# Optimization experiments

Hardware: AMD Instinct MI355X
Metric: run time of the kernel (lower is better)

The kernel has to match this reference:

```python
import jax, jax.numpy as jnp
import numpy as np

N, L, NB, D, H, DH, IN, T = 128, 512, 4, 1024, 16, 64, 1024, 512


def setup_inputs() -> dict:
    key = jax.random.key(0)
    ks = iter(jax.random.split(key, 80))

    def nrm(shape, scale=1.0):
        return jax.random.normal(next(ks), shape, jnp.float32) * scale

    sD = 1.0 / float(np.sqrt(D))
    sH = 1.0 / float(np.sqrt(DH))
    inp = {
        "x": nrm((N, IN)),
        "memories": nrm((N, L, NB, D)),
        "mask": jnp.ones((N, L), jnp.int32),
        "memory_indices": jnp.sort(jax.random.randint(next(ks), (N, L), 0, T), axis=1),
        "max_episode_steps": T,
        "We": nrm((IN, D), sD), "be": jnp.zeros((D,), jnp.float32),
        "Wq": nrm((NB, H, DH, DH), sH), "Wk": nrm((NB, H, DH, DH), sH), "Wv": nrm((NB, H, DH, DH), sH),
        "Wo": nrm((NB, D, D), sD), "bo": jnp.zeros((NB, D), jnp.float32),
        "Wfc": nrm((NB, D, D), sD), "bfc": jnp.zeros((NB, D), jnp.float32),
        "ln1_g": jnp.ones((NB, D), jnp.float32), "ln1_b": jnp.zeros((NB, D), jnp.float32),
        "ln2_g": jnp.ones((NB, D), jnp.float32), "ln2_b": jnp.zeros((NB, D), jnp.float32),
        "lnkv_g": jnp.ones((NB, D), jnp.float32), "lnkv_b": jnp.zeros((NB, D), jnp.float32),
    }
    for g in ("g1", "g2"):
        for w in ("Wr", "Ur", "Wz", "Uz", "Wg", "Ug"):
            inp[g + "_" + w] = nrm((NB, D, D), sD)
        inp[g + "_bg"] = jnp.zeros((NB, D), jnp.float32)
    return inp


def _ln(x, g, b):
    m = jnp.mean(x, -1, keepdims=True)
    v = jnp.var(x, -1, keepdims=True)
    return (x - m) / jnp.sqrt(v + 1e-5) * g + b


def _gru(x, y, Wr, Ur, Wz, Uz, Wg, Ug, bg):
    # GTrXL GRU gate (swap_inputs=False): x = residual stream, y = sublayer output
    r = jax.nn.sigmoid(y @ Wr + x @ Ur)
    z = jax.nn.sigmoid(y @ Wz + x @ Uz - bg)
    h = jnp.tanh(y @ Wg + (r * x) @ Ug)
    return (1.0 - z) * x + z * h


def reference(x, memories, mask, memory_indices, max_episode_steps,
              We, be, Wq, Wk, Wv, Wo, bo, Wfc, bfc,
              ln1_g, ln1_b, ln2_g, ln2_b, lnkv_g, lnkv_b,
              g1_Wr, g1_Ur, g1_Wz, g1_Uz, g1_Wg, g1_Ug, g1_bg,
              g2_Wr, g2_Ur, g2_Wz, g2_Uz, g2_Wg, g2_Ug, g2_bg):
    d = We.shape[1]
    nb, nh, dh, _ = Wq.shape
    n, lm = mask.shape
    h = jax.nn.relu(x @ We + be)                        # (N, D) input embedding
    # relative sinusoidal positions (newest -> oldest), as in SinusoidalPosition
    inv = 10000.0 ** (-jnp.arange(0.0, d, 2.0) / d)     # (D/2,)
    seq = jnp.arange(max_episode_steps - 1, -1, -1.0)   # (T,)
    si = seq[:, None] * inv[None, :]
    pos = jnp.concatenate([jnp.sin(si), jnp.cos(si)], -1)   # (T, D)
    mem = memories + pos[memory_indices][:, :, None, :]     # (N, L, NB, D)
    maskb = (mask == 0)[:, None, None, :]               # (N,1,1,L)
    scale = 1.0 / jnp.sqrt(jnp.float32(d))
    layer_inputs = []
    att = None
    for i in range(nb):
        layer_inputs.append(jax.lax.stop_gradient(h))
        q = h[:, None, :]                                # (N,1,D) query length 1
        q_ = _ln(q, ln1_g[i], ln1_b[i])                  # pre-LN
        kv = _ln(mem[:, :, i], lnkv_g[i], lnkv_b[i])     # key = value (shared LN)
        qh = q_.reshape(n, 1, nh, dh)
        kh = kv.reshape(n, lm, nh, dh)
        Qp = jnp.einsum('nqhd,hde->nqhe', qh, Wq[i])     # per-head projections
        Kp = jnp.einsum('nkhd,hde->nkhe', kh, Wk[i])
        Vp = jnp.einsum('nkhd,hde->nkhe', kh, Wv[i])
        energy = jnp.einsum('nqhd,nkhd->nhqk', Qp, Kp)
        energy = jnp.where(maskb, jnp.float32(-1e20), energy)
        att = jax.nn.softmax(energy * scale, axis=-1)    # scaled by sqrt(embed_dim)
        ao = jnp.einsum('nhqk,nkhd->nqhd', att, Vp).reshape(n, 1, d)
        ao = ao @ Wo[i] + bo[i]
        h1 = _gru(q, ao, g1_Wr[i], g1_Ur[i], g1_Wz[i], g1_Uz[i], g1_Wg[i], g1_Ug[i], g1_bg[i])
        h_ = _ln(h1, ln2_g[i], ln2_b[i])
        fwd = jax.nn.relu(h_ @ Wfc[i] + bfc[i])
        h = _gru(h1, fwd, g2_Wr[i], g2_Ur[i], g2_Wz[i], g2_Uz[i], g2_Wg[i], g2_Ug[i], g2_bg[i])[:, 0]
    return h, jnp.stack(layer_inputs, axis=1)            # (N,D), (N,NB,D)
```

## Files before the change

kernel.cpp:

```cpp
#include <hip/hip_runtime.h>
#include <hip/hip_bf16.h>

#define N_   128
#define L_   512
#define NB_  4
#define D_   1024
#define H_   16
#define DH_  64
#define IN_  1024
#define T_   512

#define KS_  8
#define NCV_ 32

typedef __attribute__((ext_vector_type(8))) short short8v;
typedef __attribute__((ext_vector_type(4))) float float4v;

__device__ __forceinline__ short f2bf(float f) {
  unsigned u = __float_as_uint(f);
  u += 0x7FFFu + ((u >> 16) & 1u);
  return (short)(u >> 16);
}
__device__ __forceinline__ int pack2(float a, float b) {
  return (int)(unsigned short)f2bf(a) | ((int)f2bf(b) << 16);
}

__global__ __launch_bounds__(512) void pos_kernel(float* __restrict__ pos) {
  int t = blockIdx.x;
  int j = threadIdx.x;
  float seq = (float)(T_ - 1 - t);
  float ex  = (float)(2 * j) * (1.0f / (float)D_);
  float inv = expf(-ex * 9.210340371976184f);
  float si  = seq * inv;
  pos[(size_t)t * D_ + j]        = sinf(si);
  pos[(size_t)t * D_ + 512 + j]  = cosf(si);
}

#define LDK_ 136
template<int COLW, int NC, bool HAS2>
__global__ __launch_bounds__(256) void gemm_part_t(const float* __restrict__ A1,
                                                   const float* __restrict__ B1a,
                                                   const float* __restrict__ B1b,
                                                   const float* __restrict__ A2,
                                                   const float* __restrict__ B2a,
                                                   const float* __restrict__ B2b,
                                                   float* __restrict__ Cpart) {
  constexpr int KC = 128;
  constexpr int CT = COLW / 16;
  __shared__ short As[N_ * LDK_];
  __shared__ short Bs[COLW * LDK_];
  const int tid = threadIdx.x;
  const int colg0 = blockIdx.x * COLW;
  const int k0 = blockIdx.y * KC;
  const float* B1 = B1a;
  const float* B2 = B2a;
  int col0 = colg0;
  if (NC == 2048 && colg0 >= 1024) { B1 = B1b; B2 = B2b; col0 = colg0 - 1024; }

  const int wid  = tid >> 6;
  const int lane = tid & 63;
  const int lrow = lane & 15;
  const int lk8  = (lane >> 4) * 8;
  const int wrow0 = wid * 32;

  float4v acc[2][CT];
  #pragma unroll
  for (int a = 0; a < 2; ++a)
    #pragma unroll
    for (int b = 0; b < CT; ++b)
      acc[a][b] = (float4v){0.f, 0.f, 0.f, 0.f};

  const int arow  = tid >> 1;
  const int ahalf = (tid & 1) * 64;

  #pragma unroll
  for (int pass = 0; pass < (HAS2 ? 2 : 1); ++pass) {
    const float* A = pass ? A2 : A1;
    const float* B = pass ? B2 : B1;
    if (pass) __syncthreads();
    {
      const float* ap = &A[(size_t)arow * D_ + k0 + ahalf];
      short* dst = &As[arow * LDK_ + ahalf];
      #pragma unroll
      for (int j = 0; j < 16; ++j) {
        float4 v = *(const float4*)&ap[4 * j];
        *(int2*)&dst[4 * j] = make_int2(pack2(v.x, v.y), pack2(v.z, v.w));
      }
    }
    if (COLW == 64) {
      const int bcol = tid & 63, bkq = (tid >> 6) * 32;
      int regs[16];
      #pragma unroll
      for (int j = 0; j < 16; ++j) {
        float v0 = B[(size_t)(k0 + bkq + 2 * j) * D_ + col0 + bcol];
        float v1 = B[(size_t)(k0 + bkq + 2 * j + 1) * D_ + col0 + bcol];
        regs[j] = pack2(v0, v1);
      }
      short* dst = &Bs[bcol * LDK_ + bkq];
      *(int4*)&dst[0]  = make_int4(regs[0],  regs[1],  regs[2],  regs[3]);
      *(int4*)&dst[8]  = make_int4(regs[4],  regs[5],  regs[6],  regs[7]);
      *(int4*)&dst[16] = make_int4(regs[8],  regs[9],  regs[10], regs[11]);
      *(int4*)&dst[24] = make_int4(regs[12], regs[13], regs[14], regs[15]);
    } else {
      const int bcol = tid & 31, bkq = (tid >> 5) * 16;
      int regs[8];
      #pragma unroll
      for (int j = 0; j < 8; ++j) {
        float v0 = B[(size_t)(k0 + bkq + 2 * j) * D_ + col0 + bcol];
        float v1 = B[(size_t)(k0 + bkq + 2 * j + 1) * D_ + col0 + bcol];
        regs[j] = pack2(v0, v1);
      }
      short* dst = &Bs[bcol * LDK_ + bkq];
      *(int4*)&dst[0] = make_int4(regs[0], regs[1], regs[2], regs[3]);
      *(int4*)&dst[8] = make_int4(regs[4], regs[5], regs[6], regs[7]);
    }
    __syncthreads();
    #pragma unroll
    for (int kk = 0; kk < KC; kk += 32) {
      short8v a0 = *(const short8v*)&As[(wrow0 + lrow)      * LDK_ + kk + lk8];
      short8v a1 = *(const short8v*)&As[(wrow0 + 16 + lrow) * LDK_ + kk + lk8];
      #pragma unroll
      for (int ct = 0; ct < CT; ++ct) {
        short8v bf = *(const short8v*)&Bs[(ct * 16 + lrow) * LDK_ + kk + lk8];
        acc[0][ct] = __builtin_amdgcn_mfma_f32_16x16x32_bf16(a0, bf, acc[0][ct], 0, 0, 0);
        acc[1][ct] = __builtin_amdgcn_mfma_f32_16x16x32_bf16(a1, bf, acc[1][ct], 0, 0, 0);
      }
    }
  }
  float* Cp = &Cpart[(size_t)blockIdx.y * (N_ * NC)];
  const int crow = (lane >> 4) * 4;
  const int ccol = lane & 15;
  #pragma unroll
  for (int rt = 0; rt < 2; ++rt)
    #pragma unroll
    for (int ct = 0; ct < CT; ++ct)
      #pragma unroll
      for (int j = 0; j < 4; ++j) {
        int row = wrow0 + rt * 16 + crow + j;
        int col = colg0 + ct * 16 + ccol;
        Cp[(size_t)row * NC + col] = acc[rt][ct][j];
      }
}

__device__ __forceinline__ void ln_qk_epilogue(int n, const float* v4, int tid,
                                               const float* __restrict__ lg,
                                               const float* __restrict__ lb,
                                               const float* __restrict__ Wq,
                                               const float* __restrict__ Wk,
                                               float* __restrict__ qkb,
                                               float* qln, float* Qp) {
  int c = tid * 4;
  float s = v4[0] + v4[1] + v4[2] + v4[3];
  float q = v4[0]*v4[0] + v4[1]*v4[1] + v4[2]*v4[2] + v4[3]*v4[3];
  __shared__ float sa[4], sb[4];
  #pragma unroll
  for (int o = 32; o; o >>= 1) { s += __shfl_xor(s, o, 64); q += __shfl_xor(q, o, 64); }
  if ((tid & 63) == 0) { sa[tid >> 6] = s; sb[tid >> 6] = q; }
  __syncthreads();
  s = sa[0] + sa[1] + sa[2] + sa[3];
  q = sb[0] + sb[1] + sb[2] + sb[3];
  float mean = s * (1.f / D_);
  float var  = q * (1.f / D_) - mean * mean;
  float rstd = rsqrtf(var + 1e-5f);
  #pragma unroll
  for (int j = 0; j < 4; ++j)
    qln[c + j] = (v4[j] - mean) * rstd * lg[c + j] + lb[c + j];
  __syncthreads();
  #pragma unroll
  for (int j = 0; j < 4; ++j) {
    int idx = tid + j * 256; int h = idx >> 6, e = idx & 63;
    float acc = 0.f;
    for (int d = 0; d < DH_; ++d)
      acc += qln[(h << 6) + d] * Wq[((size_t)(h << 6) + d) * DH_ + e];
    Qp[idx] = acc;
  }
  __syncthreads();
  #pragma unroll
  for (int j = 0; j < 4; ++j) {
    int idx = tid + j * 256; int h = idx >> 6, d = idx & 63;
    float acc = 0.f;
    for (int e = 0; e < DH_; ++e)
      acc += Wk[((size_t)(h << 6) + d) * DH_ + e] * Qp[(h << 6) + e];
    qkb[(size_t)n * D_ + idx] = acc * 0.03125f;
  }
}

__global__ __launch_bounds__(256) void comb_embed_lnqk(const float* __restrict__ Cp,
                                                       const float* __restrict__ bias,
                                                       const float* __restrict__ lg,
                                                       const float* __restrict__ lb,
                                                       const float* __restrict__ Wq,
                                                       const float* __restrict__ Wk,
                                                       float* __restrict__ hcur,
                                                       float* __restrict__ out_li,
                                                       float* __restrict__ qkb) {
  int n = blockIdx.x, tid = threadIdx.x, c = tid * 4;
  __shared__ float qln[D_], Qp[D_];
  float4 a4 = {0.f, 0.f, 0.f, 0.f};
  #pragma unroll
  for (int s = 0; s < KS_; ++s) {
    float4 p = *(const float4*)&Cp[(size_t)s * (N_ * D_) + (size_t)n * D_ + c];
    a4.x += p.x; a4.y += p.y; a4.z += p.z; a4.w += p.w;
  }
  float4 b4 = *(const float4*)&bias[c];
  float v[4] = {fmaxf(a4.x + b4.x, 0.f), fmaxf(a4.y + b4.y, 0.f),
                fmaxf(a4.z + b4.z, 0.f), fmaxf(a4.w + b4.w, 0.f)};
  *(float4*)&hcur[(size_t)n * D_ + c] = *(float4*)v;
  *(float4*)&out_li[((size_t)n * NB_ + 0) * D_ + c] = *(float4*)v;
  ln_qk_epilogue(n, v, tid, lg, lb, Wq, Wk, qkb, qln, Qp);
}

__global__ __launch_bounds__(256) void attn_stream(
    const float* __restrict__ mem, const float* __restrict__ pos,
    const int* __restrict__ mask, const int* __restrict__ midx,
    const float* __restrict__ qkv, const float* __restrict__ lng,
    const float* __restrict__ lnb, int blk,
    float* __restrict__ pav, float* __restrict__ pm, float* __restrict__ ps)
{
  const int n    = blockIdx.y;
  const int w    = threadIdx.x >> 6;
  const int lane = threadIdx.x & 63;
  const int vc   = blockIdx.x * 4 + w;
  const int l0   = vc * (L_ / NCV_);
  const int d0   = lane * 16;

  float g[16], bv[16], qv[16];
  #pragma unroll
  for (int j = 0; j < 4; ++j) {
    float4 t0 = *(const float4*)&lng[d0 + 4 * j];
    g[4*j+0] = t0.x; g[4*j+1] = t0.y; g[4*j+2] = t0.z; g[4*j+3] = t0.w;
    float4 t1 = *(const float4*)&lnb[d0 + 4 * j];
    bv[4*j+0] = t1.x; bv[4*j+1] = t1.y; bv[4*j+2] = t1.z; bv[4*j+3] = t1.w;
    float4 t2 = *(const float4*)&qkv[(size_t)n * D_ + d0 + 4 * j];
    qv[4*j+0] = t2.x; qv[4*j+1] = t2.y; qv[4*j+2] = t2.z; qv[4*j+3] = t2.w;
  }
  float m_run = -INFINITY, s_run = 0.f;
  float av[16];
  #pragma unroll
  for (int j = 0; j < 16; ++j) av[j] = 0.f;

  for (int l = l0; l < l0 + (L_ / NCV_); ++l) {
    if (mask[(size_t)n * L_ + l] == 0) continue;
    const float* xr = &mem[(((size_t)n * L_ + l) * NB_ + blk) * D_ + d0];
    const int tt = midx[(size_t)n * L_ + l];
    const float* pr = &pos[(size_t)tt * D_ + d0];
    float xv[16];
    #pragma unroll
    for (int j = 0; j < 4; ++j) {
      float4 a = *(const float4*)&xr[4 * j];
      float4 p = *(const float4*)&pr[4 * j];
      xv[4*j+0] = a.x + p.x; xv[4*j+1] = a.y + p.y;
      xv[4*j+2] = a.z + p.z; xv[4*j+3] = a.w + p.w;
    }
    float s1 = 0.f, s2 = 0.f;
    #pragma unroll
    for (int j = 0; j < 16; ++j) { s1 += xv[j]; s2 += xv[j] * xv[j]; }
    #pragma unroll
    for (int o = 32; o; o >>= 1) { s1 += __shfl_xor(s1, o, 64); s2 += __shfl_xor(s2, o, 64); }
    float mean = s1 * (1.f / D_);
    float var  = s2 * (1.f / D_) - mean * mean;
    float rstd = rsqrtf(var + 1e-5f);
    float e = 0.f;
    float y[16];
    #pragma unroll
    for (int j = 0; j < 16; ++j) {
      y[j] = (xv[j] - mean) * rstd * g[j] + bv[j];
      e += y[j] * qv[j];
    }
    e += __shfl_xor(e, 1, 64);
    e += __shfl_xor(e, 2, 64);
    float mn = fmaxf(m_run, e);
    float al = __expf(m_run - mn);
    float pw = __expf(e - mn);
    s_run = s_run * al + pw;
    #pragma unroll
    for (int j = 0; j < 16; ++j) av[j] = av[j] * al + pw * y[j];
    m_run = mn;
  }
  size_t base = ((size_t)n * NCV_ + vc) * D_ + d0;
  #pragma unroll
  for (int j = 0; j < 16; ++j) pav[base + j] = av[j];
  if ((lane & 3) == 0) {
    size_t mb = ((size_t)n * NCV_ + vc) * H_ + (lane >> 2);
    pm[mb] = m_run;
    ps[mb] = s_run;
  }
}

__global__ __launch_bounds__(256) void attn_fin(const float* __restrict__ pav,
                                                const float* __restrict__ pm,
                                                const float* __restrict__ ps,
                                                const float* __restrict__ Wv,
                                                float* __restrict__ tb) {
  int n = blockIdx.x, tid = threadIdx.x;
  int d0 = tid * 4; int h = tid >> 4;
  float M = -INFINITY;
  for (int c = 0; c < NCV_; ++c) M = fmaxf(M, pm[((size_t)n * NCV_ + c) * H_ + h]);
  float S = 0.f, a0 = 0.f, a1 = 0.f, a2 = 0.f, a3 = 0.f;
  if (M > -INFINITY) {
    for (int c = 0; c < NCV_; ++c) {
      float mc = pm[((size_t)n * NCV_ + c) * H_ + h];
      if (mc == -INFINITY) continue;
      float wgt = __expf(mc - M);
      S += ps[((size_t)n * NCV_ + c) * H_ + h] * wgt;
      size_t ab = ((size_t)n * NCV_ + c) * D_ + d0;
      float4 v = *(const float4*)&pav[ab];
      a0 += v.x * wgt; a1 += v.y * wgt; a2 += v.z * wgt; a3 += v.w * wgt;
    }
  }
  float inv = (S > 0.f) ? 1.f / S : 0.f;
  __shared__ float att[D_];
  att[d0 + 0] = a0 * inv; att[d0 + 1] = a1 * inv;
  att[d0 + 2] = a2 * inv; att[d0 + 3] = a3 * inv;
  __syncthreads();
  #pragma unroll
  for (int j = 0; j < 4; ++j) {
    int idx = tid + j * 256; int hh = idx >> 6, e = idx & 63;
    float acc = 0.f;
    for (int d = 0; d < DH_; ++d)
      acc += att[(hh << 6) + d] * Wv[((size_t)(hh << 6) + d) * DH_ + e];
    tb[(size_t)n * D_ + idx] = acc;
  }
}

__global__ __launch_bounds__(256) void comb_ew(const float* __restrict__ Cp,
                                               const float* __restrict__ bias,
                                               float* __restrict__ out, int mode) {
  int base = (blockIdx.x * 256 + threadIdx.x) * 4;
  int col = base & (D_ - 1);
  float4 a4 = {0.f, 0.f, 0.f, 0.f};
  #pragma unroll
  for (int s = 0; s < KS_; ++s) {
    float4 p = *(const float4*)&Cp[(size_t)s * (N_ * D_) + base];
    a4.x += p.x; a4.y += p.y; a4.z += p.z; a4.w += p.w;
  }
  float4 b4 = *(const float4*)&bias[col];
  a4.x += b4.x; a4.y += b4.y; a4.z += b4.z; a4.w += b4.w;
  if (mode == 0) {
    a4.x = fmaxf(a4.x, 0.f); a4.y = fmaxf(a4.y, 0.f);
    a4.z = fmaxf(a4.z, 0.f); a4.w = fmaxf(a4.w, 0.f);
  }
  *(float4*)&out[base] = a4;
}

__global__ __launch_bounds__(256) void comb_rz(const float* __restrict__ Cp2,
                                               const float* __restrict__ bg,
                                               const float* __restrict__ xb,
                                               float* __restrict__ rq,
                                               float* __restrict__ zb) {
  int base = (blockIdx.x * 256 + threadIdx.x) * 4;
  int row = base >> 10, col = base & (D_ - 1);
  float4 vr = {0.f, 0.f, 0.f, 0.f}, vz = {0.f, 0.f, 0.f, 0.f};
  #pragma unroll
  for (int s = 0; s < KS_; ++s) {
    size_t b = (size_t)s * (N_ * 2048) + (size_t)row * 2048 + col;
    float4 r = *(const float4*)&Cp2[b];
    float4 z = *(const float4*)&Cp2[b + 1024];
    vr.x += r.x; vr.y += r.y; vr.z += r.z; vr.w += r.w;
    vz.x += z.x; vz.y += z.y; vz.z += z.z; vz.w += z.w;
  }
  float4 x4 = *(const float4*)&xb[base];
  float4 g4 = *(const float4*)&bg[col];
  float4 ro, zo;
  ro.x = (1.f / (1.f + __expf(-vr.x))) * x4.x;
  ro.y = (1.f / (1.f + __expf(-vr.y))) * x4.y;
  ro.z = (1.f / (1.f + __expf(-vr.z))) * x4.z;
  ro.w = (1.f / (1.f + __expf(-vr.w))) * x4.w;
  zo.x = 1.f / (1.f + __expf(-(vz.x - g4.x)));
  zo.y = 1.f / (1.f + __expf(-(vz.y - g4.y)));
  zo.z = 1.f / (1.f + __expf(-(vz.z - g4.z)));
  zo.w = 1.f / (1.f + __expf(-(vz.w - g4.w)));
  *(float4*)&rq[base] = ro;
  *(float4*)&zb[base] = zo;
}

__global__ __launch_bounds__(256) void comb_h_ln(const float* __restrict__ Cp,
                                                 const float* __restrict__ zbuf,
                                                 const float* __restrict__ xb,
                                                 const float* __restrict__ lg,
                                                 const float* __restrict__ lb,
                                                 float* __restrict__ h1,
                                                 float* __restrict__ hl) {
  int n = blockIdx.x, tid = threadIdx.x, c = tid * 4;
  float4 a4 = {0.f, 0.f, 0.f, 0.f};
  #pragma unroll
  for (int ss = 0; ss < KS_; ++ss) {
    float4 p = *(const float4*)&Cp[(size_t)ss * (N_ * D_) + (size_t)n * D_ + c];
    a4.x += p.x; a4.y += p.y; a4.z += p.z; a4.w += p.w;
  }
  float4 z4 = *(const float4*)&zbuf[(size_t)n * D_ + c];
  float4 x4 = *(const float4*)&xb[(size_t)n * D_ + c];
  float v[4];
  v[0] = (1.f - z4.x) * x4.x + z4.x * tanhf(a4.x);
  v[1] = (1.f - z4.y) * x4.y + z4.y * tanhf(a4.y);
  v[2] = (1.f - z4.z) * x4.z + z4.z * tanhf(a4.z);
  v[3] = (1.f - z4.w) * x4.w + z4.w * tanhf(a4.w);
  *(float4*)&h1[(size_t)n * D_ + c] = *(float4*)v;
  float s = v[0] + v[1] + v[2] + v[3];
  float q = v[0]*v[0] + v[1]*v[1] + v[2]*v[2] + v[3]*v[3];
  __shared__ float sa[4], sb[4];
  #pragma unroll
  for (int o = 32; o; o >>= 1) { s += __shfl_xor(s, o, 64); q += __shfl_xor(q, o, 64); }
  if ((tid & 63) == 0) { sa[tid >> 6] = s; sb[tid >> 6] = q; }
  __syncthreads();
  s = sa[0] + sa[1] + sa[2] + sa[3];
  q = sb[0] + sb[1] + sb[2] + sb[3];
  float mean = s * (1.f / D_);
  float var  = q * (1.f / D_) - mean * mean;
  float rstd = rsqrtf(var + 1e-5f);
  #pragma unroll
  for (int j = 0; j < 4; ++j)
    hl[(size_t)n * D_ + c + j] = (v[j] - mean) * rstd * lg[c + j] + lb[c + j];
}

__global__ __launch_bounds__(256) void comb_h2_lnqk(const float* __restrict__ Cp,
                                                    const float* __restrict__ zbuf,
                                                    const float* __restrict__ xb,
                                                    const float* __restrict__ lg,
                                                    const float* __restrict__ lb,
                                                    const float* __restrict__ Wq,
                                                    const float* __restrict__ Wk,
                                                    float* __restrict__ hcur,
                                                    float* __restrict__ outp,
                                                    int slot,
                                                    float* __restrict__ qkb) {
  int n = blockIdx.x, tid = threadIdx.x, c = tid * 4;
  __shared__ float qln[D_], Qp[D_];
  float4 a4 = {0.f, 0.f, 0.f, 0.f};
  #pragma unroll
  for (int ss = 0; ss < KS_; ++ss) {
    float4 p = *(const float4*)&Cp[(size_t)ss * (N_ * D_) + (size_t)n * D_ + c];
    a4.x += p.x; a4.y += p.y; a4.z += p.z; a4.w += p.w;
  }
  float4 z4 = *(const float4*)&zbuf[(size_t)n * D_ + c];
  float4 x4 = *(const float4*)&xb[(size_t)n * D_ + c];
  float v[4];
  v[0] = (1.f - z4.x) * x4.x + z4.x * tanhf(a4.x);
  v[1] = (1.f - z4.y) * x4.y + z4.y * tanhf(a4.y);
  v[2] = (1.f - z4.z) * x4.z + z4.z * tanhf(a4.z);
  v[3] = (1.f - z4.w) * x4.w + z4.w * tanhf(a4.w);
  *(float4*)&hcur[(size_t)n * D_ + c] = *(float4*)v;
  size_t bi = (slot >= 0) ? (((size_t)n * NB_ + slot) * D_ + c)
                          : ((size_t)n * D_ + c);
  *(float4*)&outp[bi] = *(float4*)v;
  if (Wq != nullptr)
    ln_qk_epilogue(n, v, tid, lg, lb, Wq, Wk, qkb, qln, Qp);
}

extern "C" void kernel_launch(void* const* d_in, const int* in_sizes, int n_in,
                              void* d_out, int out_size, void* d_ws, size_t ws_size,
                              hipStream_t stream) {
  const float* x    = (const float*)d_in[0];
  const float* mem  = (const float*)d_in[1];
  const int*   mask = (const int*)d_in[2];
  const int*   midx = (const int*)d_in[3];
  const float* We   = (const float*)d_in[5];
  const float* be   = (const float*)d_in[6];
  const float* Wq   = (const float*)d_in[7];
  const float* Wk   = (const float*)d_in[8];
  const float* Wv   = (const float*)d_in[9];
  const float* Wo   = (const float*)d_in[10];
  const float* bo   = (const float*)d_in[11];
  const float* Wfc  = (const float*)d_in[12];
  const float* bfc  = (const float*)d_in[13];
  const float* ln1g = (const float*)d_in[14];
  const float* ln1b = (const float*)d_in[15];
  const float* ln2g = (const float*)d_in[16];
  const float* ln2b = (const float*)d_in[17];
  const float* lnkg = (const float*)d_in[18];
  const float* lnkb = (const float*)d_in[19];
  const float* g1w[7]; for (int j = 0; j < 7; ++j) g1w[j] = (const float*)d_in[20 + j];
  const float* g2w[7]; for (int j = 0; j < 7; ++j) g2w[j] = (const float*)d_in[27 + j];
  float* out = (float*)d_out;
  float* out_li = out + (size_t)N_ * D_;

  float* ws   = (float*)d_ws;
  float* pos  = ws; ws += (size_t)T_ * D_;
  float* hcur = ws; ws += N_ * D_;
  float* qkb  = ws; ws += N_ * D_;
  float* tb   = ws; ws += N_ * D_;
  float* ao   = ws; ws += N_ * D_;
  float* rq   = ws; ws += N_ * D_;
  float* zb   = ws; ws += N_ * D_;
  float* h1   = ws; ws += N_ * D_;
  float* hl   = ws; ws += N_ * D_;
  float* fwd  = ws; ws += N_ * D_;
  float* gpart = ws; ws += (size_t)KS_ * N_ * 2048;
  float* pav   = ws; ws += (size_t)N_ * NCV_ * D_;
  float* pm    = ws; ws += (size_t)N_ * NCV_ * H_;
  float* ps    = ws; ws += (size_t)N_ * NCV_ * H_;

  const dim3 gp(32, KS_);
  const dim3 at_grid(NCV_ / 4, N_);

  pos_kernel<<<T_, 512, 0, stream>>>(pos);

  gemm_part_t<32, 1024, false><<<gp, 256, 0, stream>>>(x, We, nullptr, nullptr, nullptr, nullptr, gpart);
  comb_embed_lnqk<<<N_, 256, 0, stream>>>(gpart, be, ln1g, ln1b, Wq, Wk, hcur, out_li, qkb);

  for (int i = 0; i < NB_; ++i) {
    size_t oD  = (size_t)i * D_;
    size_t oDD = (size_t)i * D_ * D_;
    size_t oH  = (size_t)i * H_ * DH_ * DH_;

    attn_stream<<<at_grid, 256, 0, stream>>>(mem, pos, mask, midx, qkb,
                                             lnkg + oD, lnkb + oD, i, pav, pm, ps);
    attn_fin<<<N_, 256, 0, stream>>>(pav, pm, ps, Wv + oH, tb);

    gemm_part_t<32, 1024, false><<<gp, 256, 0, stream>>>(tb, Wo + oDD, nullptr, nullptr, nullptr, nullptr, gpart);
    comb_ew<<<128, 256, 0, stream>>>(gpart, bo + oD, ao, 1);

    gemm_part_t<64, 2048, true><<<gp, 256, 0, stream>>>(ao, g1w[0] + oDD, g1w[2] + oDD,
                                                        hcur, g1w[1] + oDD, g1w[3] + oDD, gpart);
    comb_rz<<<128, 256, 0, stream>>>(gpart, g1w[6] + oD, hcur, rq, zb);
    gemm_part_t<32, 1024, true><<<gp, 256, 0, stream>>>(ao, g1w[4] + oDD, nullptr,
                                                        rq, g1w[5] + oDD, nullptr, gpart);
    comb_h_ln<<<N_, 256, 0, stream>>>(gpart, zb, hcur, ln2g + oD, ln2b + oD, h1, hl);

    gemm_part_t<32, 1024, false><<<gp, 256, 0, stream>>>(hl, Wfc + oDD, nullptr, nullptr, nullptr, nullptr, gpart);
    comb_ew<<<128, 256, 0, stream>>>(gpart, bfc + oD, fwd, 0);

    gemm_part_t<64, 2048, true><<<gp, 256, 0, stream>>>(fwd, g2w[0] + oDD, g2w[2] + oDD,
                                                        h1, g2w[1] + oDD, g2w[3] + oDD, gpart);
    comb_rz<<<128, 256, 0, stream>>>(gpart, g2w[6] + oD, h1, rq, zb);
    gemm_part_t<32, 1024, true><<<gp, 256, 0, stream>>>(fwd, g2w[4] + oDD, nullptr,
                                                        rq, g2w[5] + oDD, nullptr, gpart);

    bool last = (i == NB_ - 1);
    float* outp = last ? out : out_li;
    int slot = last ? -1 : (i + 1);
    const float* nWq = last ? nullptr : (Wq + oH + H_ * DH_ * DH_);
    const float* nWk = last ? nullptr : (Wk + oH + H_ * DH_ * DH_);
    const float* nlg = last ? nullptr : (ln1g + oD + D_);
    const float* nlb = last ? nullptr : (ln1b + oD + D_);
    comb_h2_lnqk<<<N_, 256, 0, stream>>>(gpart, zb, h1, nlg, nlb, nWq, nWk,
                                         hcur, outp, slot, qkb);
  }
}
```

Measured before the change: 802.9 us.

## Split GEMM K across two wave groups and unroll attention stream by two

The partial GEMM kernel now runs with 512 threads: two groups of four waves each take half of the 128-wide K chunk, and their accumulators are summed through shared memory before the store. The attention streaming kernel processes two memory rows per iteration so loads and reductions can overlap. It also halves the number of L-chunks per sample (NCV 32→16), giving fewer but longer blocks. Masked rows now get a large negative energy instead of being skipped. Together these aim to raise latency hiding and MFMA issue per block, at the cost of an extra shared-memory reduction, more register pressure and less grid parallelism in attention.

```diff
diff --git a/kernel.cpp b/kernel.cpp
--- a/kernel.cpp
+++ b/kernel.cpp
@@ -11,7 +11,7 @@
 #define T_   512
 
 #define KS_  8
-#define NCV_ 32
+#define NCV_ 16
 
 typedef __attribute__((ext_vector_type(8))) short short8v;
 typedef __attribute__((ext_vector_type(4))) float float4v;
@@ -38,7 +38,7 @@
 
 #define LDK_ 136
 template<int COLW, int NC, bool HAS2>
-__global__ __launch_bounds__(256) void gemm_part_t(const float* __restrict__ A1,
+__global__ __launch_bounds__(512) void gemm_part_t(const float* __restrict__ A1,
                                                    const float* __restrict__ B1a,
                                                    const float* __restrict__ B1b,
                                                    const float* __restrict__ A2,
@@ -57,11 +57,13 @@
   int col0 = colg0;
   if (NC == 2048 && colg0 >= 1024) { B1 = B1b; B2 = B2b; col0 = colg0 - 1024; }
 
-  const int wid  = tid >> 6;
-  const int lane = tid & 63;
-  const int lrow = lane & 15;
-  const int lk8  = (lane >> 4) * 8;
-  const int wrow0 = wid * 32;
+  const int w     = tid >> 6;
+  const int lane  = tid & 63;
+  const int khalf = w >> 2;
+  const int wid4  = w & 3;
+  const int wrow0 = wid4 * 32;
+  const int lrow  = lane & 15;
+  const int lk8   = (lane >> 4) * 8;
 
   float4v acc[2][CT];
   #pragma unroll
@@ -70,8 +72,8 @@
     for (int b = 0; b < CT; ++b)
       acc[a][b] = (float4v){0.f, 0.f, 0.f, 0.f};
 
-  const int arow  = tid >> 1;
-  const int ahalf = (tid & 1) * 64;
+  const int arow = tid >> 2;
+  const int aoff = (tid & 3) * 32;
 
   #pragma unroll
   for (int pass = 0; pass < (HAS2 ? 2 : 1); ++pass) {
@@ -79,30 +81,16 @@
     const float* B = pass ? B2 : B1;
     if (pass) __syncthreads();
     {
-      const float* ap = &A[(size_t)arow * D_ + k0 + ahalf];
-      short* dst = &As[arow * LDK_ + ahalf];
+      const float* ap = &A[(size_t)arow * D_ + k0 + aoff];
+      short* dst = &As[arow * LDK_ + aoff];
       #pragma unroll
-      for (int j = 0; j < 16; ++j) {
+      for (int j = 0; j < 8; ++j) {
         float4 v = *(const float4*)&ap[4 * j];
         *(int2*)&dst[4 * j] = make_int2(pack2(v.x, v.y), pack2(v.z, v.w));
       }
     }
     if (COLW == 64) {
-      const int bcol = tid & 63, bkq = (tid >> 6) * 32;
-      int regs[16];
-      #pragma unroll
-      for (int j = 0; j < 16; ++j) {
-        float v0 = B[(size_t)(k0 + bkq + 2 * j) * D_ + col0 + bcol];
-        float v1 = B[(size_t)(k0 + bkq + 2 * j + 1) * D_ + col0 + bcol];
-        regs[j] = pack2(v0, v1);
-      }
-      short* dst = &Bs[bcol * LDK_ + bkq];
-      *(int4*)&dst[0]  = make_int4(regs[0],  regs[1],  regs[2],  regs[3]);
-      *(int4*)&dst[8]  = make_int4(regs[4],  regs[5],  regs[6],  regs[7]);
-      *(int4*)&dst[16] = make_int4(regs[8],  regs[9],  regs[10], regs[11]);
-      *(int4*)&dst[24] = make_int4(regs[12], regs[13], regs[14], regs[15]);
-    } else {
-      const int bcol = tid & 31, bkq = (tid >> 5) * 16;
+      const int bcol = tid & 63, bkq = (tid >> 6) * 16;
       int regs[8];
       #pragma unroll
       for (int j = 0; j < 8; ++j) {
@@ -113,33 +101,61 @@
       short* dst = &Bs[bcol * LDK_ + bkq];
       *(int4*)&dst[0] = make_int4(regs[0], regs[1], regs[2], regs[3]);
       *(int4*)&dst[8] = make_int4(regs[4], regs[5], regs[6], regs[7]);
+    } else {
+      const int bcol = tid & 31, bkq = (tid >> 5) * 8;
+      int regs[4];
+      #pragma unroll
+      for (int j = 0; j < 4; ++j) {
+        float v0 = B[(size_t)(k0 + bkq + 2 * j) * D_ + col0 + bcol];
+        float v1 = B[(size_t)(k0 + bkq + 2 * j + 1) * D_ + col0 + bcol];
+        regs[j] = pack2(v0, v1);
+      }
+      short* dst = &Bs[bcol * LDK_ + bkq];
+      *(int4*)&dst[0] = make_int4(regs[0], regs[1], regs[2], regs[3]);
     }
     __syncthreads();
     #pragma unroll
-    for (int kk = 0; kk < KC; kk += 32) {
-      short8v a0 = *(const short8v*)&As[(wrow0 + lrow)      * LDK_ + kk + lk8];
-      short8v a1 = *(const short8v*)&As[(wrow0 + 16 + lrow) * LDK_ + kk + lk8];
+    for (int kk = 0; kk < 64; kk += 32) {
+      const int kb = khalf * 64 + kk + lk8;
+      short8v a0 = *(const short8v*)&As[(wrow0 + lrow)      * LDK_ + kb];
+      short8v a1 = *(const short8v*)&As[(wrow0 + 16 + lrow) * LDK_ + kb];
       #pragma unroll
       for (int ct = 0; ct < CT; ++ct) {
-        short8v bf = *(const short8v*)&Bs[(ct * 16 + lrow) * LDK_ + kk + lk8];
+        short8v bf = *(const short8v*)&Bs[(ct * 16 + lrow) * LDK_ + kb];
         acc[0][ct] = __builtin_amdgcn_mfma_f32_16x16x32_bf16(a0, bf, acc[0][ct], 0, 0, 0);
         acc[1][ct] = __builtin_amdgcn_mfma_f32_16x16x32_bf16(a1, bf, acc[1][ct], 0, 0, 0);
       }
     }
   }
-  float* Cp = &Cpart[(size_t)blockIdx.y * (N_ * NC)];
-  const int crow = (lane >> 4) * 4;
-  const int ccol = lane & 15;
-  #pragma unroll
-  for (int rt = 0; rt < 2; ++rt)
-    #pragma unroll
-    for (int ct = 0; ct < CT; ++ct)
+  __syncthreads();
+  float* red = (float*)As;
+  const int rbase = (wid4 * 64 + lane) * (8 * CT);
+  if (khalf == 1) {
+    #pragma unroll
+    for (int rt = 0; rt < 2; ++rt)
       #pragma unroll
-      for (int j = 0; j < 4; ++j) {
-        int row = wrow0 + rt * 16 + crow + j;
-        int col = colg0 + ct * 16 + ccol;
-        Cp[(size_t)row * NC + col] = acc[rt][ct][j];
-      }
+      for (int ct = 0; ct < CT; ++ct)
+        #pragma unroll
+        for (int j = 0; j < 4; ++j)
+          red[rbase + (rt * CT + ct) * 4 + j] = acc[rt][ct][j];
+  }
+  __syncthreads();
+  if (khalf == 0) {
+    float* Cp = &Cpart[(size_t)blockIdx.y * (N_ * NC)];
+    const int crow = (lane >> 4) * 4;
+    const int ccol = lane & 15;
+    #pragma unroll
+    for (int rt = 0; rt < 2; ++rt)
+      #pragma unroll
+      for (int ct = 0; ct < CT; ++ct)
+        #pragma unroll
+        for (int j = 0; j < 4; ++j) {
+          float v = acc[rt][ct][j] + red[rbase + (rt * CT + ct) * 4 + j];
+          int row = wrow0 + rt * 16 + crow + j;
+          int col = colg0 + ct * 16 + ccol;
+          Cp[(size_t)row * NC + col] = v;
+        }
+  }
 }
 
 __device__ __forceinline__ void ln_qk_epilogue(int n, const float* v4, int tid,
@@ -239,42 +255,58 @@
   #pragma unroll
   for (int j = 0; j < 16; ++j) av[j] = 0.f;
 
-  for (int l = l0; l < l0 + (L_ / NCV_); ++l) {
-    if (mask[(size_t)n * L_ + l] == 0) continue;
-    const float* xr = &mem[(((size_t)n * L_ + l) * NB_ + blk) * D_ + d0];
-    const int tt = midx[(size_t)n * L_ + l];
-    const float* pr = &pos[(size_t)tt * D_ + d0];
-    float xv[16];
+  for (int l = l0; l < l0 + (L_ / NCV_); l += 2) {
+    const size_t mrow = (size_t)n * L_ + l;
+    const float* xr0 = &mem[(mrow * NB_ + blk) * D_ + d0];
+    const float* xr1 = xr0 + (size_t)NB_ * D_;
+    const int mk0 = mask[mrow], mk1 = mask[mrow + 1];
+    const float* pr0 = &pos[(size_t)midx[mrow] * D_ + d0];
+    const float* pr1 = &pos[(size_t)midx[mrow + 1] * D_ + d0];
+    float x0[16], x1[16];
     #pragma unroll
     for (int j = 0; j < 4; ++j) {
-      float4 a = *(const float4*)&xr[4 * j];
-      float4 p = *(const float4*)&pr[4 * j];
-      xv[4*j+0] = a.x + p.x; xv[4*j+1] = a.y + p.y;
-      xv[4*j+2] = a.z + p.z; xv[4*j+3] = a.w + p.w;
-    }
-    float s1 = 0.f, s2 = 0.f;
-    #pragma unroll
-    for (int j = 0; j < 16; ++j) { s1 += xv[j]; s2 += xv[j] * xv[j]; }
-    #pragma unroll
-    for (int o = 32; o; o >>= 1) { s1 += __shfl_xor(s1, o, 64); s2 += __shfl_xor(s2, o, 64); }
-    float mean = s1 * (1.f / D_);
-    float var  = s2 * (1.f / D_) - mean * mean;
-    float rstd = rsqrtf(var + 1e-5f);
-    float e = 0.f;
-    float y[16];
+      float4 a = *(const float4*)&xr0[4 * j];
+      float4 p = *(const float4*)&pr0[4 * j];
+      x0[4*j+0] = a.x + p.x; x0[4*j+1] = a.y + p.y;
+      x0[4*j+2] = a.z + p.z; x0[4*j+3] = a.w + p.w;
+      float4 b = *(const float4*)&xr1[4 * j];
+      float4 q2 = *(const float4*)&pr1[4 * j];
+      x1[4*j+0] = b.x + q2.x; x1[4*j+1] = b.y + q2.y;
+      x1[4*j+2] = b.z + q2.z; x1[4*j+3] = b.w + q2.w;
+    }
+    float s1a = 0.f, s2a = 0.f, s1b = 0.f, s2b = 0.f;
     #pragma unroll
     for (int j = 0; j < 16; ++j) {
-      y[j] = (xv[j] - mean) * rstd * g[j] + bv[j];
-      e += y[j] * qv[j];
-    }
-    e += __shfl_xor(e, 1, 64);
-    e += __shfl_xor(e, 2, 64);
-    float mn = fmaxf(m_run, e);
+      s1a += x0[j]; s2a += x0[j] * x0[j];
+      s1b += x1[j]; s2b += x1[j] * x1[j];
+    }
+    #pragma unroll
+    for (int o = 32; o; o >>= 1) {
+      s1a += __shfl_xor(s1a, o, 64); s2a += __shfl_xor(s2a, o, 64);
+      s1b += __shfl_xor(s1b, o, 64); s2b += __shfl_xor(s2b, o, 64);
+    }
+    float mean0 = s1a * (1.f / D_), mean1 = s1b * (1.f / D_);
+    float rstd0 = rsqrtf(s2a * (1.f / D_) - mean0 * mean0 + 1e-5f);
+    float rstd1 = rsqrtf(s2b * (1.f / D_) - mean1 * mean1 + 1e-5f);
+    float e0 = 0.f, e1 = 0.f;
+    #pragma unroll
+    for (int j = 0; j < 16; ++j) {
+      x0[j] = (x0[j] - mean0) * rstd0 * g[j] + bv[j];
+      x1[j] = (x1[j] - mean1) * rstd1 * g[j] + bv[j];
+      e0 += x0[j] * qv[j];
+      e1 += x1[j] * qv[j];
+    }
+    e0 += __shfl_xor(e0, 1, 64); e0 += __shfl_xor(e0, 2, 64);
+    e1 += __shfl_xor(e1, 1, 64); e1 += __shfl_xor(e1, 2, 64);
+    if (!mk0) e0 = -3.125e18f;
+    if (!mk1) e1 = -3.125e18f;
+    float mn = fmaxf(m_run, fmaxf(e0, e1));
     float al = __expf(m_run - mn);
-    float pw = __expf(e - mn);
-    s_run = s_run * al + pw;
-    #pragma unroll
-    for (int j = 0; j < 16; ++j) av[j] = av[j] * al + pw * y[j];
+    float p0 = __expf(e0 - mn);
+    float p1 = __expf(e1 - mn);
+    s_run = s_run * al + p0 + p1;
+    #pragma unroll
+    for (int j = 0; j < 16; ++j) av[j] = av[j] * al + p0 * x0[j] + p1 * x1[j];
     m_run = mn;
   }
   size_t base = ((size_t)n * NCV_ + vc) * D_ + d0;
@@ -495,7 +527,7 @@
 
   pos_kernel<<<T_, 512, 0, stream>>>(pos);
 
-  gemm_part_t<32, 1024, false><<<gp, 256, 0, stream>>>(x, We, nullptr, nullptr, nullptr, nullptr, gpart);
+  gemm_part_t<32, 1024, false><<<gp, 512, 0, stream>>>(x, We, nullptr, nullptr, nullptr, nullptr, gpart);
   comb_embed_lnqk<<<N_, 256, 0, stream>>>(gpart, be, ln1g, ln1b, Wq, Wk, hcur, out_li, qkb);
 
   for (int i = 0; i < NB_; ++i) {
@@ -507,23 +539,23 @@
                                              lnkg + oD, lnkb + oD, i, pav, pm, ps);
     attn_fin<<<N_, 256, 0, stream>>>(pav, pm, ps, Wv + oH, tb);
 
-    gemm_part_t<32, 1024, false><<<gp, 256, 0, stream>>>(tb, Wo + oDD, nullptr, nullptr, nullptr, nullptr, gpart);
+    gemm_part_t<32, 1024, false><<<gp, 512, 0, stream>>>(tb, Wo + oDD, nullptr, nullptr, nullptr, nullptr, gpart);
     comb_ew<<<128, 256, 0, stream>>>(gpart, bo + oD, ao, 1);
 
-    gemm_part_t<64, 2048, true><<<gp, 256, 0, stream>>>(ao, g1w[0] + oDD, g1w[2] + oDD,
+    gemm_part_t<64, 2048, true><<<gp, 512, 0, stream>>>(ao, g1w[0] + oDD, g1w[2] + oDD,
                                                         hcur, g1w[1] + oDD, g1w[3] + oDD, gpart);
     comb_rz<<<128, 256, 0, stream>>>(gpart, g1w[6] + oD, hcur, rq, zb);
-    gemm_part_t<32, 1024, true><<<gp, 256, 0, stream>>>(ao, g1w[4] + oDD, nullptr,
+    gemm_part_t<32, 1024, true><<<gp, 512, 0, stream>>>(ao, g1w[4] + oDD, nullptr,
                                                         rq, g1w[5] + oDD, nullptr, gpart);
     comb_h_ln<<<N_, 256, 0, stream>>>(gpart, zb, hcur, ln2g + oD, ln2b + oD, h1, hl);
 
-    gemm_part_t<32, 1024, false><<<gp, 256, 0, stream>>>(hl, Wfc + oDD, nullptr, nullptr, nullptr, nullptr, gpart);
+    gemm_part_t<32, 1024, false><<<gp, 512, 0, stream>>>(hl, Wfc + oDD, nullptr, nullptr, nullptr, nullptr, gpart);
     comb_ew<<<128, 256, 0, stream>>>(gpart, bfc + oD, fwd, 0);
 
-    gemm_part_t<64, 2048, true><<<gp, 256, 0, stream>>>(fwd, g2w[0] + oDD, g2w[2] + oDD,
+    gemm_part_t<64, 2048, true><<<gp, 512, 0, stream>>>(fwd, g2w[0] + oDD, g2w[2] + oDD,
                                                         h1, g2w[1] + oDD, g2w[3] + oDD, gpart);
     comb_rz<<<128, 256, 0, stream>>>(gpart, g2w[6] + oD, h1, rq, zb);
-    gemm_part_t<32, 1024, true><<<gp, 256, 0, stream>>>(fwd, g2w[4] + oDD, nullptr,
+    gemm_part_t<32, 1024, true><<<gp, 512, 0, stream>>>(fwd, g2w[4] + oDD, nullptr,
                                                         rq, g2w[5] + oDD, nullptr, gpart);
 
     bool last = (i == NB_ - 1);
```

Result: slower. 873.3 us (+8.8%).

## Fuse split-K partial reduction and gate epilogues into next GEMM A-load

Applied to the files above, without the earlier changes.

Removes the comb_ew and comb_rz kernels by having each GEMM sum the split-K partials, add bias/relu or apply the sigmoid reset gate while loading its A tile. The z-gate sigmoid is moved into the h-combine kernels, and separate partial buffers P1/P2/P3 keep intermediate results alive. This cuts kernel launches and intermediate global writes, but every column block redundantly re-reads all 8 partial slices for its A tile, multiplying A-side memory traffic.

```diff
diff --git a/kernel.cpp b/kernel.cpp
--- a/kernel.cpp
+++ b/kernel.cpp
@@ -36,15 +36,46 @@
   pos[(size_t)t * D_ + 512 + j]  = cosf(si);
 }
 
+template<int AMODE>
+__device__ __forceinline__ float4 a_fetch(const float* __restrict__ A,
+                                          const float* __restrict__ gp,
+                                          const float* __restrict__ aux,
+                                          int row, int k) {
+  if (AMODE == 0) {
+    return *(const float4*)&A[(size_t)row * D_ + k];
+  }
+  constexpr int W = (AMODE == 3) ? 2048 : 1024;
+  float4 a = {0.f, 0.f, 0.f, 0.f};
+  #pragma unroll
+  for (int s = 0; s < KS_; ++s) {
+    float4 p = *(const float4*)&gp[(size_t)s * (N_ * W) + (size_t)row * W + k];
+    a.x += p.x; a.y += p.y; a.z += p.z; a.w += p.w;
+  }
+  if (AMODE == 1) {
+    float4 b = *(const float4*)&aux[k];
+    a.x += b.x; a.y += b.y; a.z += b.z; a.w += b.w;
+  } else if (AMODE == 2) {
+    float4 b = *(const float4*)&aux[k];
+    a.x = fmaxf(a.x + b.x, 0.f); a.y = fmaxf(a.y + b.y, 0.f);
+    a.z = fmaxf(a.z + b.z, 0.f); a.w = fmaxf(a.w + b.w, 0.f);
+  } else if (AMODE == 3) {
+    float4 xm = *(const float4*)&aux[(size_t)row * D_ + k];
+    a.x = (1.f / (1.f + __expf(-a.x))) * xm.x;
+    a.y = (1.f / (1.f + __expf(-a.y))) * xm.y;
+    a.z = (1.f / (1.f + __expf(-a.z))) * xm.z;
+    a.w = (1.f / (1.f + __expf(-a.w))) * xm.w;
+  }
+  return a;
+}
+
 #define LDK_ 136
-template<int COLW, int NC, bool HAS2>
-__global__ __launch_bounds__(256) void gemm_part_t(const float* __restrict__ A1,
-                                                   const float* __restrict__ B1a,
-                                                   const float* __restrict__ B1b,
-                                                   const float* __restrict__ A2,
-                                                   const float* __restrict__ B2a,
-                                                   const float* __restrict__ B2b,
-                                                   float* __restrict__ Cpart) {
+template<int COLW, int NC, int A1M, int A2M>
+__global__ __launch_bounds__(256) void gemm_part_t(
+    const float* __restrict__ A1, const float* __restrict__ gp1, const float* __restrict__ aux1,
+    const float* __restrict__ A2, const float* __restrict__ gp2, const float* __restrict__ aux2,
+    const float* __restrict__ B1a, const float* __restrict__ B1b,
+    const float* __restrict__ B2a, const float* __restrict__ B2b,
+    float* __restrict__ Cpart) {
   constexpr int KC = 128;
   constexpr int CT = COLW / 16;
   __shared__ short As[N_ * LDK_];
@@ -74,16 +105,16 @@
   const int ahalf = (tid & 1) * 64;
 
   #pragma unroll
-  for (int pass = 0; pass < (HAS2 ? 2 : 1); ++pass) {
-    const float* A = pass ? A2 : A1;
+  for (int pass = 0; pass < ((A2M >= 0) ? 2 : 1); ++pass) {
     const float* B = pass ? B2 : B1;
     if (pass) __syncthreads();
     {
-      const float* ap = &A[(size_t)arow * D_ + k0 + ahalf];
       short* dst = &As[arow * LDK_ + ahalf];
       #pragma unroll
       for (int j = 0; j < 16; ++j) {
-        float4 v = *(const float4*)&ap[4 * j];
+        float4 v = (pass == 0)
+            ? a_fetch<A1M>(A1, gp1, aux1, arow, k0 + ahalf + 4 * j)
+            : a_fetch<(A2M >= 0) ? A2M : 0>(A2, gp2, aux2, arow, k0 + ahalf + 4 * j);
         *(int2*)&dst[4 * j] = make_int2(pack2(v.x, v.y), pack2(v.z, v.w));
       }
     }
@@ -323,72 +354,29 @@
   }
 }
 
-__global__ __launch_bounds__(256) void comb_ew(const float* __restrict__ Cp,
-                                               const float* __restrict__ bias,
-                                               float* __restrict__ out, int mode) {
-  int base = (blockIdx.x * 256 + threadIdx.x) * 4;
-  int col = base & (D_ - 1);
-  float4 a4 = {0.f, 0.f, 0.f, 0.f};
-  #pragma unroll
-  for (int s = 0; s < KS_; ++s) {
-    float4 p = *(const float4*)&Cp[(size_t)s * (N_ * D_) + base];
-    a4.x += p.x; a4.y += p.y; a4.z += p.z; a4.w += p.w;
-  }
-  float4 b4 = *(const float4*)&bias[col];
-  a4.x += b4.x; a4.y += b4.y; a4.z += b4.z; a4.w += b4.w;
-  if (mode == 0) {
-    a4.x = fmaxf(a4.x, 0.f); a4.y = fmaxf(a4.y, 0.f);
-    a4.z = fmaxf(a4.z, 0.f); a4.w = fmaxf(a4.w, 0.f);
-  }
-  *(float4*)&out[base] = a4;
-}
-
-__global__ __launch_bounds__(256) void comb_rz(const float* __restrict__ Cp2,
-                                               const float* __restrict__ bg,
-                                               const float* __restrict__ xb,
-                                               float* __restrict__ rq,
-                                               float* __restrict__ zb) {
-  int base = (blockIdx.x * 256 + threadIdx.x) * 4;
-  int row = base >> 10, col = base & (D_ - 1);
-  float4 vr = {0.f, 0.f, 0.f, 0.f}, vz = {0.f, 0.f, 0.f, 0.f};
-  #pragma unroll
-  for (int s = 0; s < KS_; ++s) {
-    size_t b = (size_t)s * (N_ * 2048) + (size_t)row * 2048 + col;
-    float4 r = *(const float4*)&Cp2[b];
-    float4 z = *(const float4*)&Cp2[b + 1024];
-    vr.x += r.x; vr.y += r.y; vr.z += r.z; vr.w += r.w;
-    vz.x += z.x; vz.y += z.y; vz.z += z.z; vz.w += z.w;
-  }
-  float4 x4 = *(const float4*)&xb[base];
-  float4 g4 = *(const float4*)&bg[col];
-  float4 ro, zo;
-  ro.x = (1.f / (1.f + __expf(-vr.x))) * x4.x;
-  ro.y = (1.f / (1.f + __expf(-vr.y))) * x4.y;
-  ro.z = (1.f / (1.f + __expf(-vr.z))) * x4.z;
-  ro.w = (1.f / (1.f + __expf(-vr.w))) * x4.w;
-  zo.x = 1.f / (1.f + __expf(-(vz.x - g4.x)));
-  zo.y = 1.f / (1.f + __expf(-(vz.y - g4.y)));
-  zo.z = 1.f / (1.f + __expf(-(vz.z - g4.z)));
-  zo.w = 1.f / (1.f + __expf(-(vz.w - g4.w)));
-  *(float4*)&rq[base] = ro;
-  *(float4*)&zb[base] = zo;
-}
-
-__global__ __launch_bounds__(256) void comb_h_ln(const float* __restrict__ Cp,
-                                                 const float* __restrict__ zbuf,
+__global__ __launch_bounds__(256) void comb_h_ln(const float* __restrict__ CpH,
+                                                 const float* __restrict__ gpRZ,
+                                                 const float* __restrict__ bg,
                                                  const float* __restrict__ xb,
                                                  const float* __restrict__ lg,
                                                  const float* __restrict__ lb,
                                                  float* __restrict__ h1,
                                                  float* __restrict__ hl) {
   int n = blockIdx.x, tid = threadIdx.x, c = tid * 4;
-  float4 a4 = {0.f, 0.f, 0.f, 0.f};
+  float4 a4 = {0.f, 0.f, 0.f, 0.f}, zz = {0.f, 0.f, 0.f, 0.f};
   #pragma unroll
   for (int ss = 0; ss < KS_; ++ss) {
-    float4 p = *(const float4*)&Cp[(size_t)ss * (N_ * D_) + (size_t)n * D_ + c];
+    float4 p = *(const float4*)&CpH[(size_t)ss * (N_ * D_) + (size_t)n * D_ + c];
     a4.x += p.x; a4.y += p.y; a4.z += p.z; a4.w += p.w;
-  }
-  float4 z4 = *(const float4*)&zbuf[(size_t)n * D_ + c];
+    float4 zp = *(const float4*)&gpRZ[(size_t)ss * (N_ * 2048) + (size_t)n * 2048 + 1024 + c];
+    zz.x += zp.x; zz.y += zp.y; zz.z += zp.z; zz.w += zp.w;
+  }
+  float4 g4 = *(const float4*)&bg[c];
+  float4 z4;
+  z4.x = 1.f / (1.f + __expf(-(zz.x - g4.x)));
+  z4.y = 1.f / (1.f + __expf(-(zz.y - g4.y)));
+  z4.z = 1.f / (1.f + __expf(-(zz.z - g4.z)));
+  z4.w = 1.f / (1.f + __expf(-(zz.w - g4.w)));
   float4 x4 = *(const float4*)&xb[(size_t)n * D_ + c];
   float v[4];
   v[0] = (1.f - z4.x) * x4.x + z4.x * tanhf(a4.x);
@@ -413,8 +401,9 @@
     hl[(size_t)n * D_ + c + j] = (v[j] - mean) * rstd * lg[c + j] + lb[c + j];
 }
 
-__global__ __launch_bounds__(256) void comb_h2_lnqk(const float* __restrict__ Cp,
-                                                    const float* __restrict__ zbuf,
+__global__ __launch_bounds__(256) void comb_h2_lnqk(const float* __restrict__ CpH,
+                                                    const float* __restrict__ gpRZ,
+                                                    const float* __restrict__ bg,
                                                     const float* __restrict__ xb,
                                                     const float* __restrict__ lg,
                                                     const float* __restrict__ lb,
@@ -426,13 +415,20 @@
                                                     float* __restrict__ qkb) {
   int n = blockIdx.x, tid = threadIdx.x, c = tid * 4;
   __shared__ float qln[D_], Qp[D_];
-  float4 a4 = {0.f, 0.f, 0.f, 0.f};
+  float4 a4 = {0.f, 0.f, 0.f, 0.f}, zz = {0.f, 0.f, 0.f, 0.f};
   #pragma unroll
   for (int ss = 0; ss < KS_; ++ss) {
-    float4 p = *(const float4*)&Cp[(size_t)ss * (N_ * D_) + (size_t)n * D_ + c];
+    float4 p = *(const float4*)&CpH[(size_t)ss * (N_ * D_) + (size_t)n * D_ + c];
     a4.x += p.x; a4.y += p.y; a4.z += p.z; a4.w += p.w;
-  }
-  float4 z4 = *(const float4*)&zbuf[(size_t)n * D_ + c];
+    float4 zp = *(const float4*)&gpRZ[(size_t)ss * (N_ * 2048) + (size_t)n * 2048 + 1024 + c];
+    zz.x += zp.x; zz.y += zp.y; zz.z += zp.z; zz.w += zp.w;
+  }
+  float4 g4 = *(const float4*)&bg[c];
+  float4 z4;
+  z4.x = 1.f / (1.f + __expf(-(zz.x - g4.x)));
+  z4.y = 1.f / (1.f + __expf(-(zz.y - g4.y)));
+  z4.z = 1.f / (1.f + __expf(-(zz.z - g4.z)));
+  z4.w = 1.f / (1.f + __expf(-(zz.w - g4.w)));
   float4 x4 = *(const float4*)&xb[(size_t)n * D_ + c];
   float v[4];
   v[0] = (1.f - z4.x) * x4.x + z4.x * tanhf(a4.x);
@@ -479,24 +475,24 @@
   float* hcur = ws; ws += N_ * D_;
   float* qkb  = ws; ws += N_ * D_;
   float* tb   = ws; ws += N_ * D_;
-  float* ao   = ws; ws += N_ * D_;
-  float* rq   = ws; ws += N_ * D_;
-  float* zb   = ws; ws += N_ * D_;
   float* h1   = ws; ws += N_ * D_;
   float* hl   = ws; ws += N_ * D_;
-  float* fwd  = ws; ws += N_ * D_;
-  float* gpart = ws; ws += (size_t)KS_ * N_ * 2048;
-  float* pav   = ws; ws += (size_t)N_ * NCV_ * D_;
-  float* pm    = ws; ws += (size_t)N_ * NCV_ * H_;
-  float* ps    = ws; ws += (size_t)N_ * NCV_ * H_;
+  float* P1   = ws; ws += (size_t)KS_ * N_ * 1024;
+  float* P2   = ws; ws += (size_t)KS_ * N_ * 2048;
+  float* P3   = ws; ws += (size_t)KS_ * N_ * 1024;
+  float* pav  = ws; ws += (size_t)N_ * NCV_ * D_;
+  float* pm   = ws; ws += (size_t)N_ * NCV_ * H_;
+  float* ps   = ws; ws += (size_t)N_ * NCV_ * H_;
 
   const dim3 gp(32, KS_);
   const dim3 at_grid(NCV_ / 4, N_);
 
   pos_kernel<<<T_, 512, 0, stream>>>(pos);
 
-  gemm_part_t<32, 1024, false><<<gp, 256, 0, stream>>>(x, We, nullptr, nullptr, nullptr, nullptr, gpart);
-  comb_embed_lnqk<<<N_, 256, 0, stream>>>(gpart, be, ln1g, ln1b, Wq, Wk, hcur, out_li, qkb);
+  gemm_part_t<32, 1024, 0, -1><<<gp, 256, 0, stream>>>(
+      x, nullptr, nullptr, nullptr, nullptr, nullptr,
+      We, nullptr, nullptr, nullptr, P1);
+  comb_embed_lnqk<<<N_, 256, 0, stream>>>(P1, be, ln1g, ln1b, Wq, Wk, hcur, out_li, qkb);
 
   for (int i = 0; i < NB_; ++i) {
     size_t oD  = (size_t)i * D_;
@@ -507,24 +503,29 @@
                                              lnkg + oD, lnkb + oD, i, pav, pm, ps);
     attn_fin<<<N_, 256, 0, stream>>>(pav, pm, ps, Wv + oH, tb);
 
-    gemm_part_t<32, 1024, false><<<gp, 256, 0, stream>>>(tb, Wo + oDD, nullptr, nullptr, nullptr, nullptr, gpart);
-    comb_ew<<<128, 256, 0, stream>>>(gpart, bo + oD, ao, 1);
-
-    gemm_part_t<64, 2048, true><<<gp, 256, 0, stream>>>(ao, g1w[0] + oDD, g1w[2] + oDD,
-                                                        hcur, g1w[1] + oDD, g1w[3] + oDD, gpart);
-    comb_rz<<<128, 256, 0, stream>>>(gpart, g1w[6] + oD, hcur, rq, zb);
-    gemm_part_t<32, 1024, true><<<gp, 256, 0, stream>>>(ao, g1w[4] + oDD, nullptr,
-                                                        rq, g1w[5] + oDD, nullptr, gpart);
-    comb_h_ln<<<N_, 256, 0, stream>>>(gpart, zb, hcur, ln2g + oD, ln2b + oD, h1, hl);
-
-    gemm_part_t<32, 1024, false><<<gp, 256, 0, stream>>>(hl, Wfc + oDD, nullptr, nullptr, nullptr, nullptr, gpart);
-    comb_ew<<<128, 256, 0, stream>>>(gpart, bfc + oD, fwd, 0);
-
-    gemm_part_t<64, 2048, true><<<gp, 256, 0, stream>>>(fwd, g2w[0] + oDD, g2w[2] + oDD,
-                                                        h1, g2w[1] + oDD, g2w[3] + oDD, gpart);
-    comb_rz<<<128, 256, 0, stream>>>(gpart, g2w[6] + oD, h1, rq, zb);
-    gemm_part_t<32, 1024, true><<<gp, 256, 0, stream>>>(fwd, g2w[4] + oDD, nullptr,
-                                                        rq, g2w[5] + oDD, nullptr, gpart);
+    gemm_part_t<32, 1024, 0, -1><<<gp, 256, 0, stream>>>(
+        tb, nullptr, nullptr, nullptr, nullptr, nullptr,
+        Wo + oDD, nullptr, nullptr, nullptr, P1);
+
+    gemm_part_t<64, 2048, 1, 0><<<gp, 256, 0, stream>>>(
+        nullptr, P1, bo + oD, hcur, nullptr, nullptr,
+        g1w[0] + oDD, g1w[2] + oDD, g1w[1] + oDD, g1w[3] + oDD, P2);
+    gemm_part_t<32, 1024, 1, 3><<<gp, 256, 0, stream>>>(
+        nullptr, P1, bo + oD, nullptr, P2, hcur,
+        g1w[4] + oDD, nullptr, g1w[5] + oDD, nullptr, P3);
+    comb_h_ln<<<N_, 256, 0, stream>>>(P3, P2, g1w[6] + oD, hcur,
+                                      ln2g + oD, ln2b + oD, h1, hl);
+
+    gemm_part_t<32, 1024, 0, -1><<<gp, 256, 0, stream>>>(
+        hl, nullptr, nullptr, nullptr, nullptr, nullptr,
+        Wfc + oDD, nullptr, nullptr, nullptr, P1);
+
+    gemm_part_t<64, 2048, 2, 0><<<gp, 256, 0, stream>>>(
+        nullptr, P1, bfc + oD, h1, nullptr, nullptr,
+        g2w[0] + oDD, g2w[2] + oDD, g2w[1] + oDD, g2w[3] + oDD, P2);
+    gemm_part_t<32, 1024, 2, 3><<<gp, 256, 0, stream>>>(
+        nullptr, P1, bfc + oD, nullptr, P2, h1,
+        g2w[4] + oDD, nullptr, g2w[5] + oDD, nullptr, P3);
 
     bool last = (i == NB_ - 1);
     float* outp = last ? out : out_li;
@@ -533,7 +534,7 @@
     const float* nWk = last ? nullptr : (Wk + oH + H_ * DH_ * DH_);
     const float* nlg = last ? nullptr : (ln1g + oD + D_);
     const float* nlb = last ? nullptr : (ln1b + oD + D_);
-    comb_h2_lnqk<<<N_, 256, 0, stream>>>(gpart, zb, h1, nlg, nlb, nWq, nWk,
-                                         hcur, outp, slot, qkb);
-  }
-}
+    comb_h2_lnqk<<<N_, 256, 0, stream>>>(P3, P2, g2w[6] + oD, h1, nlg, nlb,
+                                         nWq, nWk, hcur, outp, slot, qkb);
+  }
+}
```

Result: slower. 1.549 ms (+93.0%).
